# Kernel tuning notes

Measured on AMD Instinct MI355X. Metric: run time of the kernel, lower is better.

## Reference

```python
import jax, jax.numpy as jnp
import numpy as np

N = 100000; E = 1600000; B = 256; T = 200
EMB = 128; GH = 64; H = 128; DUR = 32; TDIM = 4
IN1 = 2 + EMB + TDIM  # 134


def setup_inputs() -> dict:
    key = jax.random.key(0)
    ks = jax.random.split(key, 20)
    f32 = jnp.float32
    D_IN = EMB + DUR  # 160 lstm input
    return dict(
        x_coords=jax.random.normal(ks[0], (N, 2), f32),
        temporal_features=jax.random.normal(ks[1], (N, TDIM), f32),
        edge_index=jax.random.randint(ks[2], (2, E), 0, N),
        edge_weight=jnp.ones((E,), f32),
        seq=jax.random.randint(ks[3], (B, T), 0, N),
        durations=jax.random.uniform(ks[4], (B, T), f32, 0.0, 30.0),
        lengths=jax.random.randint(ks[5], (B,), 1, T + 1),
        node_emb=jax.random.normal(ks[6], (N, EMB), f32) * 0.02,
        gcn1_W=jax.random.normal(ks[7], (IN1, GH), f32) / np.sqrt(IN1),
        gcn1_b=jnp.zeros((GH,), f32),
        gcn2_W=jax.random.normal(ks[8], (GH, EMB), f32) / np.sqrt(GH),
        gcn2_b=jnp.zeros((EMB,), f32),
        dur_W1=jax.random.normal(ks[9], (1, 16), f32),
        dur_b1=jnp.zeros((16,), f32),
        dur_W2=jax.random.normal(ks[10], (16, DUR), f32) * 0.25,
        dur_b2=jnp.zeros((DUR,), f32),
        lstm_Wih_f=jax.random.normal(ks[11], (4 * H, D_IN), f32) / np.sqrt(D_IN),
        lstm_Whh_f=jax.random.normal(ks[12], (4 * H, H), f32) / np.sqrt(H),
        lstm_b_f=jnp.zeros((4 * H,), f32),
        lstm_Wih_b=jax.random.normal(ks[13], (4 * H, D_IN), f32) / np.sqrt(D_IN),
        lstm_Whh_b=jax.random.normal(ks[14], (4 * H, H), f32) / np.sqrt(H),
        lstm_b_b=jnp.zeros((4 * H,), f32),
        attn_W=jax.random.normal(ks[15], (2 * H, 1), f32) / np.sqrt(2 * H),
        attn_b=jnp.zeros((1,), f32),
        fc_W=jax.random.normal(ks[16], (2 * H, N), f32) / np.sqrt(2 * H),
        fc_b=jnp.zeros((N,), f32),
    )


def gcn_conv(x, W, b, edge_index, edge_weight, n):
    # PyG GCNConv: linear -> symmetric-normalized scatter-add with self-loops -> +bias
    row, col = edge_index[0], edge_index[1]
    loop = jnp.arange(n)
    row = jnp.concatenate([row, loop])
    col = jnp.concatenate([col, loop])
    ew = jnp.concatenate([edge_weight, jnp.ones((n,), x.dtype)])
    deg = jax.ops.segment_sum(ew, col, num_segments=n)
    dis = jnp.where(deg > 0, jax.lax.rsqrt(jnp.maximum(deg, 1e-12)), 0.0)
    norm = dis[row] * ew * dis[col]                 # [E+N]
    xw = x @ W                                      # [N, out]
    out = jax.ops.segment_sum(norm[:, None] * xw[row], col, num_segments=n)
    return out + b


def reverse_padded(x, lengths):
    # reverse each sequence within its valid length (packed-sequence semantics)
    t = jnp.arange(x.shape[1])[None, :]
    idx = jnp.where(t < lengths[:, None], lengths[:, None] - 1 - t, t)
    return jnp.take_along_axis(x, idx[:, :, None], axis=1)


def lstm_dir(x, Wih, Whh, b, mask):
    # x: [B,T,D]; mask: [B,T]; torch gate order i,f,g,o; padded steps freeze state, output 0
    Bz = x.shape[0]
    Hh = Whh.shape[1]
    xg = jnp.einsum('btd,gd->btg', x, Wih) + b      # [B,T,4H]

    def step(carry, inp):
        h, c = carry
        xg_t, m_t = inp
        g = xg_t + h @ Whh.T
        i, f, gg, o = jnp.split(g, 4, axis=-1)
        c_new = jax.nn.sigmoid(f) * c + jax.nn.sigmoid(i) * jnp.tanh(gg)
        h_new = jax.nn.sigmoid(o) * jnp.tanh(c_new)
        m = m_t[:, None]
        return (jnp.where(m, h_new, h), jnp.where(m, c_new, c)), jnp.where(m, h_new, 0.0)

    init = (jnp.zeros((Bz, Hh), x.dtype), jnp.zeros((Bz, Hh), x.dtype))
    _, out = jax.lax.scan(step, init, (xg.swapaxes(0, 1), mask.swapaxes(0, 1)))
    return out.swapaxes(0, 1)                        # [B,T,H]


def reference(x_coords, edge_index, seq, durations, lengths, temporal_features, edge_weight,
              node_emb, gcn1_W, gcn1_b, gcn2_W, gcn2_b,
              dur_W1, dur_b1, dur_W2, dur_b2,
              lstm_Wih_f, lstm_Whh_f, lstm_b_f, lstm_Wih_b, lstm_Whh_b, lstm_b_b,
              attn_W, attn_b, fc_W, fc_b):
    n = x_coords.shape[0]
    feats = jnp.concatenate([x_coords, node_emb, temporal_features], axis=1)  # [N,134]
    z = jax.nn.relu(gcn_conv(feats, gcn1_W, gcn1_b, edge_index, edge_weight, n))
    z = gcn_conv(z, gcn2_W, gcn2_b, edge_index, edge_weight, n)               # [N,EMB]
    seq_emb = z[seq]                                                          # [B,T,EMB]
    dur = jnp.log1p(durations)[..., None]                                     # [B,T,1]
    dur_emb = jax.nn.relu(dur @ dur_W1 + dur_b1) @ dur_W2 + dur_b2            # [B,T,DUR]
    x = jnp.concatenate([seq_emb, dur_emb], axis=-1)                          # [B,T,160]
    mask = jnp.arange(x.shape[1])[None, :] < lengths[:, None]                 # [B,T]
    out_f = lstm_dir(x, lstm_Wih_f, lstm_Whh_f, lstm_b_f, mask)
    out_b = reverse_padded(lstm_dir(reverse_padded(x, lengths), lstm_Wih_b, lstm_Whh_b, lstm_b_b, mask), lengths)
    lstm_out = jnp.concatenate([out_f, out_b], axis=-1)                       # [B,T,2H]
    scores = (lstm_out @ attn_W)[..., 0] + attn_b[0]                          # [B,T]
    scores = jnp.where(mask, scores, -jnp.inf)
    w = jax.nn.softmax(scores, axis=1)[..., None]
    context = jnp.sum(lstm_out * w, axis=1)                                   # [B,2H]
    return context @ fc_W + fc_b                                              # [B,N]
```

## Files before the change

kernel.cpp:

```cpp
#include <hip/hip_runtime.h>
#include <math.h>

#define TSEQ_MAX 256

typedef float v2f __attribute__((ext_vector_type(2)));

__device__ __forceinline__ float sigmf(float x){ return 1.f/(1.f+__expf(-x)); }
__device__ __forceinline__ float tanh_f(float x){ return 1.f - 2.f/(__expf(2.f*x)+1.f); }

__global__ void k_deg_init(float* deg, int N){
    int i = blockIdx.x*256 + threadIdx.x;
    if (i < N) deg[i] = 1.0f;
}
__global__ void k_deg_acc(const int* __restrict__ ei, const float* __restrict__ ew, float* deg, int E){
    int e = blockIdx.x*256 + threadIdx.x;
    if (e < E) atomicAdd(&deg[ei[E + e]], ew[e]);
}
__global__ void k_dis(float* deg, int N){
    int i = blockIdx.x*256 + threadIdx.x;
    if (i < N){ float d = deg[i]; deg[i] = (d > 0.f) ? rsqrtf(fmaxf(d, 1e-12f)) : 0.f; }
}

__global__ void k_count(const int* __restrict__ ei, int* __restrict__ cnt, int E){
    int e = blockIdx.x*256 + threadIdx.x;
    if (e < E) atomicAdd(&cnt[ei[E + e]], 1);
}

__global__ __launch_bounds__(256) void k_scan1(const int* __restrict__ cnt, int* __restrict__ base,
        int* __restrict__ partials, int N){
    __shared__ int sh[256];
    int tid = threadIdx.x;
    int i0 = blockIdx.x*1024 + tid*4;
    int v0=0,v1=0,v2=0,v3=0;
    if (i0+0 < N) v0 = cnt[i0+0];
    if (i0+1 < N) v1 = cnt[i0+1];
    if (i0+2 < N) v2 = cnt[i0+2];
    if (i0+3 < N) v3 = cnt[i0+3];
    int tsum = v0+v1+v2+v3;
    sh[tid] = tsum;
    __syncthreads();
    for (int off = 1; off < 256; off <<= 1){
        int val = (tid >= off) ? sh[tid-off] : 0;
        __syncthreads();
        sh[tid] += val;
        __syncthreads();
    }
    int excl = sh[tid] - tsum;
    if (i0+0 < N) base[i0+0] = excl;
    if (i0+1 < N) base[i0+1] = excl + v0;
    if (i0+2 < N) base[i0+2] = excl + v0 + v1;
    if (i0+3 < N) base[i0+3] = excl + v0 + v1 + v2;
    if (tid == 255) partials[blockIdx.x] = sh[255];
}
__global__ __launch_bounds__(128) void k_scan2(int* partials, int nb){
    __shared__ int sh[128];
    int tid = threadIdx.x;
    int v = (tid < nb) ? partials[tid] : 0;
    sh[tid] = v;
    __syncthreads();
    for (int off = 1; off < 128; off <<= 1){
        int val = (tid >= off) ? sh[tid-off] : 0;
        __syncthreads();
        sh[tid] += val;
        __syncthreads();
    }
    if (tid < nb) partials[tid] = sh[tid] - v;
}
__global__ void k_scan3(int* base, int* cursor, const int* __restrict__ partials, int N, int E){
    int i = blockIdx.x*256 + threadIdx.x;
    if (i < N){
        int v = base[i] + partials[i >> 10];
        base[i] = v; cursor[i] = v;
    }
    if (i == N) base[N] = E;
}
__global__ void k_scatter(const int* __restrict__ ei, const float* __restrict__ ew,
        const float* __restrict__ dis, int* cursor, int2* __restrict__ sorted, int E){
    int e = blockIdx.x*256 + threadIdx.x;
    if (e < E){
        int r = ei[e], c = ei[E + e];
        float nrm = dis[r] * ew[e] * dis[c];
        int pos = atomicAdd(&cursor[c], 1);
        sorted[pos] = make_int2(r, __float_as_int(nrm));
    }
}

__global__ __launch_bounds__(256) void k_xw1(const float* __restrict__ xc, const float* __restrict__ te,
        const float* __restrict__ emb, const float* __restrict__ W1,
        float* __restrict__ xw1, int N){
    __shared__ float Ws[134*64];
    __shared__ float fs[4][136];
    int tid = threadIdx.x;
    for (int i = tid; i < 134*64; i += 256) Ws[i] = W1[i];
    int sub = tid >> 6, lane = tid & 63;
    int node = blockIdx.x*4 + sub;
    if (node < N){
        fs[sub][2+lane]      = emb[node*128 + lane];
        fs[sub][2+64+lane]   = emb[node*128 + 64 + lane];
        if (lane < 2) fs[sub][lane]       = xc[node*2 + lane];
        if (lane < 4) fs[sub][130 + lane] = te[node*4 + lane];
    }
    __syncthreads();
    if (node < N){
        float acc = 0.f;
        #pragma unroll 2
        for (int k = 0; k < 134; k++) acc += fs[sub][k] * Ws[k*64 + lane];
        xw1[node*64 + lane] = acc;
    }
}

__global__ __launch_bounds__(256) void k_gather1(const int2* __restrict__ sorted, const int* __restrict__ base,
        const float* __restrict__ dis, const float* __restrict__ xw1, const float* __restrict__ b1,
        float* __restrict__ out1, int N){
    int node = blockIdx.x*4 + (threadIdx.x >> 6);
    int lane = threadIdx.x & 63;
    if (node >= N) return;
    int s = base[node], e_end = base[node+1];
    float d = dis[node];
    float acc = b1[lane] + d*d*xw1[(size_t)node*64 + lane];
    for (int e = s; e < e_end; e++){
        int2 pr = sorted[e];
        acc += __int_as_float(pr.y) * xw1[(size_t)pr.x*64 + lane];
    }
    out1[(size_t)node*64 + lane] = acc;
}

__global__ __launch_bounds__(256) void k_xw2(const float* __restrict__ out1, const float* __restrict__ W2,
        float* __restrict__ xw2, int N){
    __shared__ float Ws[64*128];
    __shared__ float zs[2][68];
    int tid = threadIdx.x;
    for (int i = tid; i < 64*128; i += 256) Ws[i] = W2[i];
    int sub = tid >> 7, lane = tid & 127;
    int node = blockIdx.x*2 + sub;
    if (node < N && lane < 64) zs[sub][lane] = fmaxf(out1[node*64 + lane], 0.f);
    __syncthreads();
    if (node < N){
        float acc = 0.f;
        #pragma unroll 4
        for (int k = 0; k < 64; k++) acc += zs[sub][k] * Ws[k*128 + lane];
        xw2[(size_t)node*128 + lane] = acc;
    }
}

__global__ __launch_bounds__(256) void k_gather2(const int2* __restrict__ sorted, const int* __restrict__ base,
        const float* __restrict__ dis, const float* __restrict__ xw2, const float* __restrict__ b2,
        float* __restrict__ z, int N){
    int node = blockIdx.x*2 + (threadIdx.x >> 7);
    int lane = threadIdx.x & 127;
    if (node >= N) return;
    int s = base[node], e_end = base[node+1];
    float d = dis[node];
    float acc = b2[lane] + d*d*xw2[(size_t)node*128 + lane];
    for (int e = s; e < e_end; e++){
        int2 pr = sorted[e];
        acc += __int_as_float(pr.y) * xw2[(size_t)pr.x*128 + lane];
    }
    z[(size_t)node*128 + lane] = acc;
}

__global__ void k_build_x(const float* __restrict__ z, const int* __restrict__ seq,
        const float* __restrict__ dur, const float* __restrict__ dW1, const float* __restrict__ db1,
        const float* __restrict__ dW2, const float* __restrict__ db2, float* __restrict__ x){
    int row = blockIdx.x;
    int tid = threadIdx.x;
    if (tid < 128){
        int node = seq[row];
        x[row*160 + tid] = z[node*128 + tid];
    } else if (tid < 160){
        int jj = tid - 128;
        float ld = log1pf(dur[row]);
        float acc = db2[jj];
        #pragma unroll
        for (int hh = 0; hh < 16; hh++){
            float hv = fmaxf(ld * dW1[hh] + db1[hh], 0.f);
            acc += hv * dW2[hh*32 + jj];
        }
        x[row*160 + tid] = acc;
    }
}

__global__ void k_transpose_wih(const float* __restrict__ Wf, const float* __restrict__ Wb,
        float* __restrict__ Tf, float* __restrict__ Tb){
    int idx = blockIdx.x*256 + threadIdx.x;
    if (idx < 512*160){
        int g = idx / 160, k = idx % 160;
        Tf[k*512 + g] = Wf[idx];
        Tb[k*512 + g] = Wb[idx];
    }
}

#define MT 64
#define NT 128
#define KC 16
__global__ __launch_bounds__(256) void k_gemm(const float* __restrict__ A, const float* __restrict__ B,
        const float* __restrict__ bias, float* __restrict__ C, int M, int Nn, int K){
    __shared__ float As[KC][MT+4];
    __shared__ float Bs[KC][NT+4];
    int tid = threadIdx.x;
    int n0 = blockIdx.x * NT;
    int m0 = blockIdx.y * MT;
    int tn = tid & 31;
    int tm = tid >> 5;
    v2f acc[8][2];
    #pragma unroll
    for (int i = 0; i < 8; i++){ acc[i][0] = (v2f){0.f,0.f}; acc[i][1] = (v2f){0.f,0.f}; }

    for (int kt = 0; kt < K; kt += KC){
        {
            int m = tid >> 2, q = tid & 3;
            float4 a4 = *(const float4*)(A + (size_t)(m0+m)*K + kt + q*4);
            As[q*4+0][m] = a4.x; As[q*4+1][m] = a4.y; As[q*4+2][m] = a4.z; As[q*4+3][m] = a4.w;
        }
        {
            #pragma unroll
            for (int i = 0; i < 2; i++){
                int idx = tid*2 + i;
                int r = idx >> 5, c4 = idx & 31;
                int col = n0 + c4*4;
                float4 bv = make_float4(0.f,0.f,0.f,0.f);
                if (col < Nn) bv = *(const float4*)(B + (size_t)(kt+r)*Nn + col);
                *(float4*)(&Bs[r][c4*4]) = bv;
            }
        }
        __syncthreads();
        #pragma unroll
        for (int k = 0; k < KC; k++){
            float4 b4 = *(const float4*)(&Bs[k][tn*4]);
            v2f b01 = (v2f){b4.x, b4.y};
            v2f b23 = (v2f){b4.z, b4.w};
            float4 a0 = *(const float4*)(&As[k][tm*8]);
            float4 a1 = *(const float4*)(&As[k][tm*8+4]);
            float av[8] = {a0.x,a0.y,a0.z,a0.w,a1.x,a1.y,a1.z,a1.w};
            #pragma unroll
            for (int i = 0; i < 8; i++){
                v2f ai = (v2f){av[i], av[i]};
                acc[i][0] = __builtin_elementwise_fma(ai, b01, acc[i][0]);
                acc[i][1] = __builtin_elementwise_fma(ai, b23, acc[i][1]);
            }
        }
        __syncthreads();
    }
    int col = n0 + tn*4;
    if (col < Nn){
        float4 bb = *(const float4*)(bias + col);
        #pragma unroll
        for (int i = 0; i < 8; i++){
            int row = m0 + tm*8 + i;
            float4 o = make_float4(acc[i][0].x+bb.x, acc[i][0].y+bb.y, acc[i][1].x+bb.z, acc[i][1].y+bb.w);
            *(float4*)(C + (size_t)row*Nn + col) = o;
        }
    }
}

__global__ __launch_bounds__(512) void k_sortjobs(const int* __restrict__ lengths,
        int* __restrict__ jobs, int* __restrict__ counter){
    __shared__ int keys[512];
    __shared__ int vals[512];
    int tid = threadIdx.x;
    keys[tid] = -lengths[tid >> 1];
    vals[tid] = tid;
    __syncthreads();
    for (int k = 2; k <= 512; k <<= 1){
        for (int jj = k >> 1; jj > 0; jj >>= 1){
            int ixj = tid ^ jj;
            if (ixj > tid){
                bool up = ((tid & k) == 0);
                int k0 = keys[tid], k1 = keys[ixj];
                if ((k0 > k1) == up){
                    keys[tid] = k1; keys[ixj] = k0;
                    int v0 = vals[tid]; vals[tid] = vals[ixj]; vals[ixj] = v0;
                }
            }
            __syncthreads();
        }
    }
    jobs[tid] = vals[tid];
    if (tid == 0) *counter = 0;
}

__global__ __launch_bounds__(512, 1) void k_lstm(const float* __restrict__ xg_f, const float* __restrict__ xg_b,
        const float* __restrict__ Whh_f, const float* __restrict__ Whh_b,
        const int* __restrict__ lengths, const int* __restrict__ jobs, int* __restrict__ counter,
        float* __restrict__ lstm_out, int T){
    __shared__ int job_s;
    int j = threadIdx.x;
    if (j == 0) job_s = atomicAdd(counter, 1);
    __syncthreads();
    int job = jobs[job_s];
    int b = job >> 1, dir = job & 1;
    const float* xg  = dir ? xg_b  : xg_f;
    const float* Whh = dir ? Whh_b : Whh_f;
    int len = lengths[b];
    __shared__ __align__(16) float h[128];
    __shared__ float g[512];
    v2f w[64];
    const v2f* wrow = (const v2f*)(Whh + j*128);
    #pragma unroll
    for (int k = 0; k < 64; k++) w[k] = wrow[k];
    if (j < 128) h[j] = 0.f;
    float c = 0.f;
    const float* xgb = xg + (size_t)b*T*512 + j;
    float* lob = lstm_out + (size_t)b*T*256 + dir*128 + j;
    int t0 = dir ? (len-1) : 0;
    float xg_next = xgb[(size_t)t0*512];
    __syncthreads();
    for (int s = 0; s < len; s++){
        int t = dir ? (len-1-s) : s;
        float xgv = xg_next;
        if (s+1 < len){
            int tn = dir ? (len-2-s) : (s+1);
            xg_next = xgb[(size_t)tn*512];
        }
        const float4* h4 = (const float4*)h;
        v2f p0 = (v2f){0.f,0.f}, p1 = (v2f){0.f,0.f}, p2 = (v2f){0.f,0.f}, p3 = (v2f){0.f,0.f};
        #pragma unroll
        for (int k = 0; k < 32; k += 2){
            float4 ha = h4[k+0];
            float4 hb = h4[k+1];
            p0 = __builtin_elementwise_fma(w[2*k+0], (v2f){ha.x,ha.y}, p0);
            p1 = __builtin_elementwise_fma(w[2*k+1], (v2f){ha.z,ha.w}, p1);
            p2 = __builtin_elementwise_fma(w[2*k+2], (v2f){hb.x,hb.y}, p2);
            p3 = __builtin_elementwise_fma(w[2*k+3], (v2f){hb.z,hb.w}, p3);
        }
        g[j] = xgv + (((p0.x+p0.y)+(p1.x+p1.y)) + ((p2.x+p2.y)+(p3.x+p3.y)));
        __syncthreads();
        if (j < 128){
            float gi = g[j], gf = g[128+j], gg = g[256+j], go = g[384+j];
            float cn = sigmf(gf)*c + sigmf(gi)*tanh_f(gg);
            float hn = sigmf(go)*tanh_f(cn);
            c = cn;
            h[j] = hn;
            lob[(size_t)t*256] = hn;
        }
        __syncthreads();
    }
}

__global__ __launch_bounds__(256) void k_attn(const float* __restrict__ lstm_out,
        const float* __restrict__ attn_W, const int* __restrict__ lengths,
        float* __restrict__ context, int T){
    int b = blockIdx.x;
    int tid = threadIdx.x;
    int len = lengths[b];
    __shared__ float sc[TSEQ_MAX];
    __shared__ float red[8];
    int lane = tid & 63, wv = tid >> 6;
    float a0 = attn_W[lane], a1 = attn_W[64+lane], a2 = attn_W[128+lane], a3 = attn_W[192+lane];
    for (int t = wv; t < len; t += 4){
        const float* r = lstm_out + ((size_t)b*T + t)*256;
        float p = r[lane]*a0 + r[64+lane]*a1 + r[128+lane]*a2 + r[192+lane]*a3;
        #pragma unroll
        for (int o = 32; o > 0; o >>= 1) p += __shfl_down(p, o);
        if (lane == 0) sc[t] = p;
    }
    __syncthreads();
    float v = (tid < len) ? sc[tid] : -INFINITY;
    float m = v;
    #pragma unroll
    for (int o = 32; o > 0; o >>= 1) m = fmaxf(m, __shfl_down(m, o));
    if (lane == 0) red[wv] = m;
    __syncthreads();
    float M4 = fmaxf(fmaxf(red[0],red[1]), fmaxf(red[2],red[3]));
    float e = (tid < len) ? __expf(v - M4) : 0.f;
    float ss = e;
    #pragma unroll
    for (int o = 32; o > 0; o >>= 1) ss += __shfl_down(ss, o);
    if (lane == 0) red[4+wv] = ss;
    __syncthreads();
    float S = red[4]+red[5]+red[6]+red[7];
    sc[tid] = e / S;
    __syncthreads();
    float acc = 0.f;
    for (int t = 0; t < len; t++) acc += sc[t] * lstm_out[((size_t)b*T + t)*256 + tid];
    context[b*256 + tid] = acc;
}

extern "C" void kernel_launch(void* const* d_in, const int* in_sizes, int n_in,
                              void* d_out, int out_size, void* d_ws, size_t ws_size,
                              hipStream_t stream) {
    const float* x_coords  = (const float*)d_in[0];
    const float* temporal  = (const float*)d_in[1];
    const int*   edge_idx  = (const int*)  d_in[2];
    const float* edge_w    = (const float*)d_in[3];
    const int*   seq       = (const int*)  d_in[4];
    const float* durations = (const float*)d_in[5];
    const int*   lengths   = (const int*)  d_in[6];
    const float* node_emb  = (const float*)d_in[7];
    const float* gcn1_W    = (const float*)d_in[8];
    const float* gcn1_b    = (const float*)d_in[9];
    const float* gcn2_W    = (const float*)d_in[10];
    const float* gcn2_b    = (const float*)d_in[11];
    const float* dur_W1    = (const float*)d_in[12];
    const float* dur_b1    = (const float*)d_in[13];
    const float* dur_W2    = (const float*)d_in[14];
    const float* dur_b2    = (const float*)d_in[15];
    const float* Wih_f     = (const float*)d_in[16];
    const float* Whh_f     = (const float*)d_in[17];
    const float* b_f       = (const float*)d_in[18];
    const float* Wih_b     = (const float*)d_in[19];
    const float* Whh_b     = (const float*)d_in[20];
    const float* b_b       = (const float*)d_in[21];
    const float* attn_W    = (const float*)d_in[22];
    const float* fc_W      = (const float*)d_in[24];
    const float* fc_b      = (const float*)d_in[25];
    float* out = (float*)d_out;
    float* ws  = (float*)d_ws;

    const int N  = in_sizes[0] / 2;
    const int E  = in_sizes[2] / 2;
    const int B  = in_sizes[6];
    const int T  = in_sizes[4] / B;
    const int BT = B * T;

    float* xg_f     = ws + 0;
    float* xg_b     = ws + 26214400;
    float* xbuf     = ws + 52428800;
    float* lstm_out = ws + 60620800;
    float* context  = ws + 73728000;
    float* WihT_f   = ws + 73793536;
    float* WihT_b   = ws + 73875456;

    int* jobs    = (int*)context;
    int* counter = (int*)context + 512;

    float* dis  = ws + 0;
    float* xw1  = ws + 100352;
    float* out1 = ws + 6500352;
    float* xw2  = ws + 12900352;
    float* zbuf = ws + 25700352;
    int2*  sorted   = (int2*)(ws + 38500352);
    int*   cnt      = (int*) (ws + 41700352);
    int*   base     = (int*) (ws + 41800352);
    int*   cursor   = (int*) (ws + 41900356);
    int*   partials = (int*) (ws + 42000356);

    const int SCAN_BLOCKS = (N + 1023) / 1024;

    k_sortjobs<<<dim3(1), dim3(512), 0, stream>>>(lengths, jobs, counter);

    k_deg_init<<<dim3((N+255)/256), dim3(256), 0, stream>>>(dis, N);
    k_deg_acc <<<dim3((E+255)/256), dim3(256), 0, stream>>>(edge_idx, edge_w, dis, E);
    k_dis     <<<dim3((N+255)/256), dim3(256), 0, stream>>>(dis, N);

    hipMemsetAsync(cnt, 0, (size_t)N*sizeof(int), stream);
    k_count  <<<dim3((E+255)/256), dim3(256), 0, stream>>>(edge_idx, cnt, E);
    k_scan1  <<<dim3(SCAN_BLOCKS), dim3(256), 0, stream>>>(cnt, base, partials, N);
    k_scan2  <<<dim3(1), dim3(128), 0, stream>>>(partials, SCAN_BLOCKS);
    k_scan3  <<<dim3((N+256)/256), dim3(256), 0, stream>>>(base, cursor, partials, N, E);
    k_scatter<<<dim3((E+255)/256), dim3(256), 0, stream>>>(edge_idx, edge_w, dis, cursor, sorted, E);

    k_xw1    <<<dim3((N+3)/4), dim3(256), 0, stream>>>(x_coords, temporal, node_emb, gcn1_W, xw1, N);
    k_gather1<<<dim3((N+3)/4), dim3(256), 0, stream>>>(sorted, base, dis, xw1, gcn1_b, out1, N);

    k_xw2    <<<dim3((N+1)/2), dim3(256), 0, stream>>>(out1, gcn2_W, xw2, N);
    k_gather2<<<dim3((N+1)/2), dim3(256), 0, stream>>>(sorted, base, dis, xw2, gcn2_b, zbuf, N);

    k_build_x<<<dim3(BT), dim3(192), 0, stream>>>(zbuf, seq, durations, dur_W1, dur_b1, dur_W2, dur_b2, xbuf);

    k_transpose_wih<<<dim3(320), dim3(256), 0, stream>>>(Wih_f, Wih_b, WihT_f, WihT_b);
    k_gemm<<<dim3(512/NT, BT/MT), dim3(256), 0, stream>>>(xbuf, WihT_f, b_f, xg_f, BT, 512, 160);
    k_gemm<<<dim3(512/NT, BT/MT), dim3(256), 0, stream>>>(xbuf, WihT_b, b_b, xg_b, BT, 512, 160);

    k_lstm<<<dim3(2*B), dim3(512), 0, stream>>>(xg_f, xg_b, Whh_f, Whh_b, lengths, jobs, counter, lstm_out, T);

    k_attn<<<dim3(B), dim3(256), 0, stream>>>(lstm_out, attn_W, lengths, context, T);

    k_gemm<<<dim3((N + NT - 1)/NT, B/MT), dim3(256), 0, stream>>>(context, fc_W, fc_b, out, B, N, 256);
}
```

Baseline: 1.812 ms.

## Aggregate before projecting in second GCN layer and unroll edge gathers

The second GCN layer now aggregates the ReLU'd 64-wide hidden features over neighbors first and only then applies the 64x128 projection plus bias. Before, it projected to 128 wide and then gathered 128-wide rows. This halves the bytes moved per edge in the dominant gather, and ReLU is fused into the gather. The gather loop is unrolled by four to keep more independent loads in flight. The projection kernel now processes eight nodes per block, so the weight tile loaded into shared memory is reused more.

```diff
diff --git a/kernel.cpp b/kernel.cpp
--- a/kernel.cpp
+++ b/kernel.cpp
@@ -109,54 +109,63 @@
     }
 }
 
-__global__ __launch_bounds__(256) void k_gather1(const int2* __restrict__ sorted, const int* __restrict__ base,
-        const float* __restrict__ dis, const float* __restrict__ xw1, const float* __restrict__ b1,
-        float* __restrict__ out1, int N){
+template<bool RELU>
+__global__ __launch_bounds__(256) void k_gather64(const int2* __restrict__ sorted, const int* __restrict__ base,
+        const float* __restrict__ dis, const float* __restrict__ src, const float* __restrict__ b,
+        float* __restrict__ outp, int N){
     int node = blockIdx.x*4 + (threadIdx.x >> 6);
     int lane = threadIdx.x & 63;
     if (node >= N) return;
     int s = base[node], e_end = base[node+1];
     float d = dis[node];
-    float acc = b1[lane] + d*d*xw1[(size_t)node*64 + lane];
-    for (int e = s; e < e_end; e++){
+    float self = src[(size_t)node*64 + lane];
+    if (RELU) self = fmaxf(self, 0.f);
+    float acc = d*d*self;
+    if (!RELU) acc += b[lane];
+    int e = s;
+    for (; e + 4 <= e_end; e += 4){
+        int2 p0 = sorted[e+0];
+        int2 p1 = sorted[e+1];
+        int2 p2 = sorted[e+2];
+        int2 p3 = sorted[e+3];
+        float v0 = src[(size_t)p0.x*64 + lane];
+        float v1 = src[(size_t)p1.x*64 + lane];
+        float v2 = src[(size_t)p2.x*64 + lane];
+        float v3 = src[(size_t)p3.x*64 + lane];
+        if (RELU){ v0=fmaxf(v0,0.f); v1=fmaxf(v1,0.f); v2=fmaxf(v2,0.f); v3=fmaxf(v3,0.f); }
+        acc += __int_as_float(p0.y)*v0 + __int_as_float(p1.y)*v1
+             + __int_as_float(p2.y)*v2 + __int_as_float(p3.y)*v3;
+    }
+    for (; e < e_end; e++){
         int2 pr = sorted[e];
-        acc += __int_as_float(pr.y) * xw1[(size_t)pr.x*64 + lane];
-    }
-    out1[(size_t)node*64 + lane] = acc;
-}
-
-__global__ __launch_bounds__(256) void k_xw2(const float* __restrict__ out1, const float* __restrict__ W2,
-        float* __restrict__ xw2, int N){
+        float v = src[(size_t)pr.x*64 + lane];
+        if (RELU) v = fmaxf(v, 0.f);
+        acc += __int_as_float(pr.y)*v;
+    }
+    outp[(size_t)node*64 + lane] = acc;
+}
+
+__global__ __launch_bounds__(256) void k_proj(const float* __restrict__ agg, const float* __restrict__ W2,
+        const float* __restrict__ b2, float* __restrict__ z, int N){
     __shared__ float Ws[64*128];
     __shared__ float zs[2][68];
     int tid = threadIdx.x;
     for (int i = tid; i < 64*128; i += 256) Ws[i] = W2[i];
     int sub = tid >> 7, lane = tid & 127;
-    int node = blockIdx.x*2 + sub;
-    if (node < N && lane < 64) zs[sub][lane] = fmaxf(out1[node*64 + lane], 0.f);
-    __syncthreads();
-    if (node < N){
-        float acc = 0.f;
-        #pragma unroll 4
-        for (int k = 0; k < 64; k++) acc += zs[sub][k] * Ws[k*128 + lane];
-        xw2[(size_t)node*128 + lane] = acc;
-    }
-}
-
-__global__ __launch_bounds__(256) void k_gather2(const int2* __restrict__ sorted, const int* __restrict__ base,
-        const float* __restrict__ dis, const float* __restrict__ xw2, const float* __restrict__ b2,
-        float* __restrict__ z, int N){
-    int node = blockIdx.x*2 + (threadIdx.x >> 7);
-    int lane = threadIdx.x & 127;
-    if (node >= N) return;
-    int s = base[node], e_end = base[node+1];
-    float d = dis[node];
-    float acc = b2[lane] + d*d*xw2[(size_t)node*128 + lane];
-    for (int e = s; e < e_end; e++){
-        int2 pr = sorted[e];
-        acc += __int_as_float(pr.y) * xw2[(size_t)pr.x*128 + lane];
-    }
-    z[(size_t)node*128 + lane] = acc;
+    float bb = b2[lane];
+    #pragma unroll
+    for (int p = 0; p < 4; p++){
+        int node = blockIdx.x*8 + p*2 + sub;
+        __syncthreads();
+        if (node < N && lane < 64) zs[sub][lane] = agg[(size_t)node*64 + lane];
+        __syncthreads();
+        if (node < N){
+            float acc = bb;
+            #pragma unroll 4
+            for (int k = 0; k < 64; k++) acc += zs[sub][k] * Ws[k*128 + lane];
+            z[(size_t)node*128 + lane] = acc;
+        }
+    }
 }
 
 __global__ void k_build_x(const float* __restrict__ z, const int* __restrict__ seq,
@@ -427,7 +436,7 @@
     float* dis  = ws + 0;
     float* xw1  = ws + 100352;
     float* out1 = ws + 6500352;
-    float* xw2  = ws + 12900352;
+    float* agg  = ws + 12900352;
     float* zbuf = ws + 25700352;
     int2*  sorted   = (int2*)(ws + 38500352);
     int*   cnt      = (int*) (ws + 41700352);
@@ -450,11 +459,11 @@
     k_scan3  <<<dim3((N+256)/256), dim3(256), 0, stream>>>(base, cursor, partials, N, E);
     k_scatter<<<dim3((E+255)/256), dim3(256), 0, stream>>>(edge_idx, edge_w, dis, cursor, sorted, E);
 
-    k_xw1    <<<dim3((N+3)/4), dim3(256), 0, stream>>>(x_coords, temporal, node_emb, gcn1_W, xw1, N);
-    k_gather1<<<dim3((N+3)/4), dim3(256), 0, stream>>>(sorted, base, dis, xw1, gcn1_b, out1, N);
-
-    k_xw2    <<<dim3((N+1)/2), dim3(256), 0, stream>>>(out1, gcn2_W, xw2, N);
-    k_gather2<<<dim3((N+1)/2), dim3(256), 0, stream>>>(sorted, base, dis, xw2, gcn2_b, zbuf, N);
+    k_xw1<<<dim3((N+3)/4), dim3(256), 0, stream>>>(x_coords, temporal, node_emb, gcn1_W, xw1, N);
+    k_gather64<false><<<dim3((N+3)/4), dim3(256), 0, stream>>>(sorted, base, dis, xw1, gcn1_b, out1, N);
+
+    k_gather64<true><<<dim3((N+3)/4), dim3(256), 0, stream>>>(sorted, base, dis, out1, nullptr, agg, N);
+    k_proj<<<dim3((N+7)/8), dim3(256), 0, stream>>>(agg, gcn2_W, gcn2_b, zbuf, N);
 
     k_build_x<<<dim3(BT), dim3(192), 0, stream>>>(zbuf, seq, durations, dur_W1, dur_b1, dur_W2, dur_b2, xbuf);
 
```

Measured after the change: 1.502 ms. -17.1%, faster.
